# Optimization experiments

Measured on AMD Instinct MI355X. Metric: run time of the kernel, lower is better.

## Reference

```python
import jax, jax.numpy as jnp
import numpy as np

N, C_IN, C_OUT, P, W, H = 32, 32, 16, 4, 16, 16
D = P * P
EPS = 1e-6


def squash(s, axis=-1):
    # v = ||s||^2/(1+||s||^2) * s/||s||, eps-stabilized as in the repo (eps=1e-6)
    n2 = jnp.sum(s * s, axis=axis, keepdims=True)
    n = jnp.sqrt(n2)
    return (n2 / (1.0 + n2)) * s / (n + EPS)


def setup_inputs() -> dict:
    key = jax.random.key(0)
    k1, k2, k3 = jax.random.split(key, 3)
    l = jax.random.normal(k1, (N, C_IN, D, W, H), jnp.float32)
    g = jax.random.normal(k2, (N, C_OUT, D), jnp.float32)
    weight = jax.random.normal(k3, (1, C_IN, 1, C_OUT, P, P), jnp.float32)
    return {"l": l, "g": g, "weight": weight, "num_iters": 3}


def reference(l, g, weight, num_iters):
    n, c, d, w, h = l.shape
    p = weight.shape[-1]
    c_out = weight.shape[3]
    # (N, C, D, W, H) -> (N, C, W*H, P, P)
    lp = jnp.transpose(l, (0, 1, 3, 4, 2)).reshape(n, c, w * h, p, p)
    # votes: pose matmul against per-(in,out) transform matrices
    # v[n,c,s,o] = lp[n,c,s] @ weight[0,c,0,o]   -> (N, C, WH, C_out, P, P)
    v = jnp.einsum('ncsij,cojk->ncsoik', lp, weight[0, :, 0])
    M = c * w * h
    v = v.reshape(n, M, c_out, d)          # (N, M, C_out, D)
    g = g[:, None, :, :]                    # (N, 1, C_out, D)
    # dynamic routing, logits initialized from agreement with the prior global capsule g
    b = jnp.sum(v * g, axis=-1, keepdims=True)   # (N, M, C_out, 1)
    cc = None
    for _ in range(num_iters):
        cc = jax.nn.softmax(b, axis=1)           # attention over input votes M
        g = squash(jnp.sum(cc * v, axis=1, keepdims=True))  # (N, 1, C_out, D)
        b = b + jnp.sum(v * g, axis=-1, keepdims=True)
    a = jnp.squeeze(cc, -1)   # (N, M, C_out)
    g = jnp.squeeze(g, 1)     # (N, C_out, D)
    return a, g
```

## Files before the change

### kernel.cpp

```cpp
#include <hip/hip_runtime.h>
#include <math.h>

#define N_   32
#define CIN  32
#define COUT 16
#define D_   16
#define S_   256
#define M_   (CIN * S_)

#define LOG2E 1.4426950408889634f

#define PROW 20
#define PIDX(n, c, o) ((((size_t)(n) * CIN + (c)) * COUT + (o)) * PROW)

#define WS_PB0 0
#define WS_PB1 (N_ * CIN * COUT * PROW)
#define WS_G1  (2 * N_ * CIN * COUT * PROW)

#define SW(s) ((((s) & 3)) ^ (((s) >> 2) & 3))

__device__ __forceinline__ void stage_tile(const float* __restrict__ gsrc,
                                           float* ls, int tid) {
  const float4* src = (const float4*)gsrc;
#pragma unroll
  for (int j = 0; j < 4; j++) {
    int f = ((tid & 3) << 6) + (tid >> 2) + (j << 8);
    float4 val = src[f];
    int dd = f >> 6;
    int u  = f & 63;
    int chunk = dd >> 2, lo = dd & 3;
    float vv[4] = {val.x, val.y, val.z, val.w};
#pragma unroll
    for (int m = 0; m < 4; m++) {
      int s = (u << 2) + m;
      int p = chunk ^ SW(s);
      ls[(s << 4) + (p << 2) + lo] = vv[m];
    }
  }
}

__device__ __forceinline__ void read_lp(const float* ls, int s, float* lp) {
  const float4* row = (const float4*)(ls + (s << 4));
  int sw = SW(s);
#pragma unroll
  for (int c = 0; c < 4; c++) {
    float4 q = row[c ^ sw];
    lp[c * 4 + 0] = q.x; lp[c * 4 + 1] = q.y;
    lp[c * 4 + 2] = q.z; lp[c * 4 + 3] = q.w;
  }
}

__device__ __forceinline__ float dot16(const float* a, const float* b) {
  float a0 = 0.f, a1 = 0.f, a2 = 0.f, a3 = 0.f;
#pragma unroll
  for (int k = 0; k < 4; k++) {
    a0 = fmaf(a[k],      b[k],      a0);
    a1 = fmaf(a[4 + k],  b[4 + k],  a1);
    a2 = fmaf(a[8 + k],  b[8 + k],  a2);
    a3 = fmaf(a[12 + k], b[12 + k], a3);
  }
  return (a0 + a1) + (a2 + a3);
}

__global__ __launch_bounds__(256, 3) void pass_kernel(
    const float* __restrict__ l, const float* __restrict__ wgt,
    const float* __restrict__ gprev, const float* __restrict__ part_in,
    float* __restrict__ gstore, float* __restrict__ part_out,
    float* __restrict__ edump, int mode) {
  const int bid = blockIdx.x;
  const int n = bid >> 5;
  const int c = bid & 31;
  const int tid = threadIdx.x;
  const int o = tid & 15;
  const int strip = tid >> 4;

  __shared__ float ls[D_ * S_];
  __shared__ float red[4][18][16];
  __shared__ float red2[18][16];
  __shared__ float hd[16][20];

  if (mode && tid < 64) {
    const int ho = tid & 15, hs = tid >> 4;
    float H[18];
#pragma unroll
    for (int f = 0; f < 17; f++) H[f] = 0.f;
    H[17] = -INFINITY;
#pragma unroll 2
    for (int q = 0; q < 8; q++) {
      const float* r = part_in + PIDX(n, hs + 4 * q, ho);
      const float4* r4 = (const float4*)r;
#pragma unroll
      for (int i = 0; i < 4; i++) {
        float4 v = r4[i];
        H[i * 4 + 0] += v.x; H[i * 4 + 1] += v.y;
        H[i * 4 + 2] += v.z; H[i * 4 + 3] += v.w;
      }
      H[16] += r[16];
      H[17] = fmaxf(H[17], r[17]);
    }
#pragma unroll
    for (int off = 16; off <= 32; off <<= 1) {
#pragma unroll
      for (int f = 0; f < 17; f++) H[f] += __shfl_xor(H[f], off);
      H[17] = fmaxf(H[17], __shfl_xor(H[17], off));
    }
    if (tid < 16) {
      float inv = 1.0f / H[16], n2 = 0.f, Sg[16];
#pragma unroll
      for (int d = 0; d < 16; d++) { Sg[d] = H[d] * inv; n2 = fmaf(Sg[d], Sg[d], n2); }
      float coef = n2 / ((1.f + n2) * (sqrtf(n2) + 1e-6f));
      float4* hq = (float4*)hd[tid];
#pragma unroll
      for (int i = 0; i < 4; i++)
        hq[i] = make_float4(coef * Sg[i * 4 + 0], coef * Sg[i * 4 + 1],
                            coef * Sg[i * 4 + 2], coef * Sg[i * 4 + 3]);
      hd[tid][16] = H[17];
    }
  }

  stage_tile(l + ((size_t)(n * CIN + c)) * D_ * S_, ls, tid);

  float Greg[16];
  {
    const float4* gp = (const float4*)(gprev + (n * COUT + o) * 16);
#pragma unroll
    for (int i = 0; i < 4; i++) {
      float4 u = gp[i];
      Greg[i * 4 + 0] = u.x; Greg[i * 4 + 1] = u.y;
      Greg[i * 4 + 2] = u.z; Greg[i * 4 + 3] = u.w;
    }
  }

  __syncthreads();

  float shift = 0.f;
  if (mode) {
    const float4* hq = (const float4*)hd[o];
#pragma unroll
    for (int i = 0; i < 4; i++) {
      float4 v = hq[i];
      Greg[i * 4 + 0] += v.x; Greg[i * 4 + 1] += v.y;
      Greg[i * 4 + 2] += v.z; Greg[i * 4 + 3] += v.w;
    }
    shift = hd[o][16];
    if (mode == 1 && c == 0 && tid < 16) {
      float* gs = gstore + (n * COUT + tid) * 16;
      const float4* hp = (const float4*)hd[tid];
      const float4* gp = (const float4*)(gprev + (n * COUT + tid) * 16);
      float4* g4 = (float4*)gs;
#pragma unroll
      for (int i = 0; i < 4; i++) {
        float4 a = gp[i], b = hp[i];
        g4[i] = make_float4(a.x + b.x, a.y + b.y, a.z + b.z, a.w + b.w);
      }
    }
  }

  float WG[16];
  {
    float wreg[16];
    const float4* wp = (const float4*)(wgt + (c * COUT + o) * 16);
#pragma unroll
    for (int i = 0; i < 4; i++) {
      float4 t = wp[i];
      wreg[i * 4 + 0] = t.x; wreg[i * 4 + 1] = t.y;
      wreg[i * 4 + 2] = t.z; wreg[i * 4 + 3] = t.w;
    }
#pragma unroll
    for (int i = 0; i < 4; i++)
#pragma unroll
      for (int j = 0; j < 4; j++) {
        float acc = 0.f;
#pragma unroll
        for (int k = 0; k < 4; k++)
          acc = fmaf(wreg[j * 4 + k], Greg[i * 4 + k], acc);
        WG[i * 4 + j] = acc * LOG2E;
      }
  }

  float se = 0.f, bmx = -INFINITY, E[16];
#pragma unroll
  for (int d = 0; d < 16; d++) E[d] = 0.f;

#pragma unroll 4
  for (int it = 0; it < 16; it++) {
    float lp[16];
    read_lp(ls, strip + (it << 4), lp);
    float b = dot16(lp, WG) - shift;
    float e = exp2f(b);
    if (mode == 2) {
      edump[((size_t)(n * M_ + c * S_ + strip + (it << 4))) * COUT + o] = e;
    }
    bmx = fmaxf(bmx, b);
    se += e;
#pragma unroll
    for (int d = 0; d < 16; d++) E[d] = fmaf(e, lp[d], E[d]);
  }

#pragma unroll
  for (int off = 16; off <= 32; off <<= 1) {
    se += __shfl_xor(se, off);
    bmx = fmaxf(bmx, __shfl_xor(bmx, off));
#pragma unroll
    for (int d = 0; d < 16; d++) E[d] += __shfl_xor(E[d], off);
  }

  const int w = tid >> 6;
  if ((tid & 63) < 16) {
#pragma unroll
    for (int d = 0; d < 16; d++) red[w][d][o] = E[d];
    red[w][16][o] = se;
    red[w][17][o] = bmx;
  }
  __syncthreads();

  for (int p = tid; p < 288; p += 256) {
    int f = p >> 4, oo = p & 15;
    float v0 = red[0][f][oo], v1 = red[1][f][oo];
    float v2 = red[2][f][oo], v3 = red[3][f][oo];
    red2[f][oo] = (f == 17) ? fmaxf(fmaxf(v0, v1), fmaxf(v2, v3))
                            : ((v0 + v1) + (v2 + v3));
  }
  __syncthreads();

  if (tid < 16) {
    float wt[16];
    const float4* wp = (const float4*)(wgt + (c * COUT + tid) * 16);
#pragma unroll
    for (int i = 0; i < 4; i++) {
      float4 t = wp[i];
      wt[i * 4 + 0] = t.x; wt[i * 4 + 1] = t.y;
      wt[i * 4 + 2] = t.z; wt[i * 4 + 3] = t.w;
    }
    float Et[16];
#pragma unroll
    for (int d = 0; d < 16; d++) Et[d] = red2[d][tid];
    float* p0 = part_out + PIDX(n, c, tid);
    float4* p4 = (float4*)p0;
#pragma unroll
    for (int i = 0; i < 4; i++) {
      float s0 = 0.f, s1 = 0.f, s2 = 0.f, s3 = 0.f;
#pragma unroll
      for (int j = 0; j < 4; j++) {
        s0 = fmaf(Et[i * 4 + j], wt[j * 4 + 0], s0);
        s1 = fmaf(Et[i * 4 + j], wt[j * 4 + 1], s1);
        s2 = fmaf(Et[i * 4 + j], wt[j * 4 + 2], s2);
        s3 = fmaf(Et[i * 4 + j], wt[j * 4 + 3], s3);
      }
      p4[i] = make_float4(s0, s1, s2, s3);
    }
    p0[16] = red2[16][tid];
    p0[17] = red2[17][tid] + shift;
  }
}

__global__ __launch_bounds__(256, 4) void a_kernel(
    const float* __restrict__ part, float* __restrict__ a_out,
    float* __restrict__ g_out) {
  const int bid = blockIdx.x;
  const int n = bid >> 6;
  const int chunk = bid & 63;
  const int tid = threadIdx.x;

  __shared__ float sinv[16];

  if (tid < 16) {
    float se = 0.f;
    if (chunk == 0) {
      float S[16];
#pragma unroll
      for (int d = 0; d < 16; d++) S[d] = 0.f;
#pragma unroll 4
      for (int c = 0; c < CIN; c++) {
        const float* r = part + PIDX(n, c, tid);
        const float4* r4 = (const float4*)r;
#pragma unroll
        for (int i = 0; i < 4; i++) {
          float4 v = r4[i];
          S[i * 4 + 0] += v.x; S[i * 4 + 1] += v.y;
          S[i * 4 + 2] += v.z; S[i * 4 + 3] += v.w;
        }
        se += r[16];
      }
      float inv = 1.0f / se, n2 = 0.f;
#pragma unroll
      for (int d = 0; d < 16; d++) { S[d] *= inv; n2 = fmaf(S[d], S[d], n2); }
      float coef = n2 / ((1.f + n2) * (sqrtf(n2) + 1e-6f));
      float* go = g_out + (n * COUT + tid) * 16;
#pragma unroll
      for (int d = 0; d < 16; d++) go[d] = coef * S[d];
      sinv[tid] = inv;
    } else {
#pragma unroll 8
      for (int c = 0; c < CIN; c++) se += part[PIDX(n, c, tid) + 16];
      sinv[tid] = 1.0f / se;
    }
  }
  __syncthreads();

  float4* pv = (float4*)(a_out + (size_t)n * (M_ * COUT) + (size_t)chunk * 2048);
#pragma unroll
  for (int r = 0; r < 2; r++) {
    int i4 = tid + (r << 8);
    int o0 = (i4 & 3) << 2;
    float4 v = pv[i4];
    v.x *= sinv[o0 + 0];
    v.y *= sinv[o0 + 1];
    v.z *= sinv[o0 + 2];
    v.w *= sinv[o0 + 3];
    pv[i4] = v;
  }
}

extern "C" void kernel_launch(void* const* d_in, const int* in_sizes, int n_in,
                              void* d_out, int out_size, void* d_ws, size_t ws_size,
                              hipStream_t stream) {
  const float* l = (const float*)d_in[0];
  const float* g = (const float*)d_in[1];
  const float* w = (const float*)d_in[2];

  float* out = (float*)d_out;
  float* ws = (float*)d_ws;
  float* a_out = out;
  float* g_out = out + (size_t)N_ * M_ * COUT;

  float* PB0 = ws + WS_PB0;
  float* PB1 = ws + WS_PB1;
  float* G1  = ws + WS_G1;

  pass_kernel<<<N_ * CIN, 256, 0, stream>>>(l, w, g, nullptr, nullptr, PB0,
                                            nullptr, 0);
  pass_kernel<<<N_ * CIN, 256, 0, stream>>>(l, w, g, PB0, G1, PB1,
                                            nullptr, 1);
  pass_kernel<<<N_ * CIN, 256, 0, stream>>>(l, w, G1, PB1, nullptr, PB0,
                                            a_out, 2);
  a_kernel<<<N_ * 64, 256, 0, stream>>>(PB0, a_out, g_out);
}
```

Before: 119.8 us.

## Process two input channels per block with prefetch of the second tile

Each pass block now handles two input channels (c0 and c0+16), halving the grid. The second channel's tile is loaded into registers while the first is being swept, then written to shared memory after the first reduction. This hides global load latency and amortizes the per-block head reduction (mode>0) over two channels. The a_kernel likewise processes twice as many elements per block. The cost is fewer blocks (512 on a large GPU, possibly under-filling it) and higher register pressure.

```diff
diff --git a/kernel.cpp b/kernel.cpp
--- a/kernel.cpp
+++ b/kernel.cpp
@@ -19,17 +19,23 @@
 
 #define SW(s) ((((s) & 3)) ^ (((s) >> 2) & 3))
 
-__device__ __forceinline__ void stage_tile(const float* __restrict__ gsrc,
-                                           float* ls, int tid) {
+__device__ __forceinline__ void stage_load(const float* __restrict__ gsrc,
+                                           int tid, float4* vals) {
   const float4* src = (const float4*)gsrc;
+#pragma unroll
+  for (int j = 0; j < 4; j++)
+    vals[j] = src[((tid & 3) << 6) + (tid >> 2) + (j << 8)];
+}
+
+__device__ __forceinline__ void stage_store(float* ls, int tid,
+                                            const float4* vals) {
 #pragma unroll
   for (int j = 0; j < 4; j++) {
     int f = ((tid & 3) << 6) + (tid >> 2) + (j << 8);
-    float4 val = src[f];
     int dd = f >> 6;
     int u  = f & 63;
     int chunk = dd >> 2, lo = dd & 3;
-    float vv[4] = {val.x, val.y, val.z, val.w};
+    float vv[4] = {vals[j].x, vals[j].y, vals[j].z, vals[j].w};
 #pragma unroll
     for (int m = 0; m < 4; m++) {
       int s = (u << 2) + m;
@@ -61,6 +67,101 @@
   }
   return (a0 + a1) + (a2 + a3);
 }
+
+__device__ __forceinline__ void make_WG(const float* __restrict__ wgt,
+                                        int c, int o, const float* Greg,
+                                        float* WG) {
+  float wreg[16];
+  const float4* wp = (const float4*)(wgt + (c * COUT + o) * 16);
+#pragma unroll
+  for (int i = 0; i < 4; i++) {
+    float4 t = wp[i];
+    wreg[i * 4 + 0] = t.x; wreg[i * 4 + 1] = t.y;
+    wreg[i * 4 + 2] = t.z; wreg[i * 4 + 3] = t.w;
+  }
+#pragma unroll
+  for (int i = 0; i < 4; i++)
+#pragma unroll
+    for (int j = 0; j < 4; j++) {
+      float acc = 0.f;
+#pragma unroll
+      for (int k = 0; k < 4; k++)
+        acc = fmaf(wreg[j * 4 + k], Greg[i * 4 + k], acc);
+      WG[i * 4 + j] = acc * LOG2E;
+    }
+}
+
+__device__ __forceinline__ void sweep(const float* ls, const float* WG,
+                                      float shift, int strip, int doDump,
+                                      float* __restrict__ edp,
+                                      float& se, float& bmx, float* E) {
+  se = 0.f; bmx = -INFINITY;
+#pragma unroll
+  for (int d = 0; d < 16; d++) E[d] = 0.f;
+#pragma unroll 4
+  for (int it = 0; it < 16; it++) {
+    float lp[16];
+    read_lp(ls, strip + (it << 4), lp);
+    float b = dot16(lp, WG) - shift;
+    float e = exp2f(b);
+    if (doDump) edp[(size_t)(it << 4) * COUT] = e;
+    bmx = fmaxf(bmx, b);
+    se += e;
+#pragma unroll
+    for (int d = 0; d < 16; d++) E[d] = fmaf(e, lp[d], E[d]);
+  }
+#pragma unroll
+  for (int off = 16; off <= 32; off <<= 1) {
+    se += __shfl_xor(se, off);
+    bmx = fmaxf(bmx, __shfl_xor(bmx, off));
+#pragma unroll
+    for (int d = 0; d < 16; d++) E[d] += __shfl_xor(E[d], off);
+  }
+}
+
+__device__ __forceinline__ void tail_store(const float* __restrict__ wgt,
+                                           int c, int o,
+                                           float (*red2)[16],
+                                           float* __restrict__ part_out,
+                                           int n, float shift) {
+  float wt[16];
+  const float4* wp = (const float4*)(wgt + (c * COUT + o) * 16);
+#pragma unroll
+  for (int i = 0; i < 4; i++) {
+    float4 t = wp[i];
+    wt[i * 4 + 0] = t.x; wt[i * 4 + 1] = t.y;
+    wt[i * 4 + 2] = t.z; wt[i * 4 + 3] = t.w;
+  }
+  float Et[16];
+#pragma unroll
+  for (int d = 0; d < 16; d++) Et[d] = red2[d][o];
+  float* p0 = part_out + PIDX(n, c, o);
+  float4* p4 = (float4*)p0;
+#pragma unroll
+  for (int i = 0; i < 4; i++) {
+    float s0 = 0.f, s1 = 0.f, s2 = 0.f, s3 = 0.f;
+#pragma unroll
+    for (int j = 0; j < 4; j++) {
+      s0 = fmaf(Et[i * 4 + j], wt[j * 4 + 0], s0);
+      s1 = fmaf(Et[i * 4 + j], wt[j * 4 + 1], s1);
+      s2 = fmaf(Et[i * 4 + j], wt[j * 4 + 2], s2);
+      s3 = fmaf(Et[i * 4 + j], wt[j * 4 + 3], s3);
+    }
+    p4[i] = make_float4(s0, s1, s2, s3);
+  }
+  p0[16] = red2[16][o];
+  p0[17] = red2[17][o] + shift;
+}
+
+#define MERGE_STORE(w_, o_, E_, se_, bmx_)           \
+  do {                                               \
+    if ((tid & 63) < 16) {                           \
+      _Pragma("unroll")                              \
+      for (int d = 0; d < 16; d++) red[w_][d][o_] = E_[d]; \
+      red[w_][16][o_] = se_;                         \
+      red[w_][17][o_] = bmx_;                        \
+    }                                                \
+  } while (0)
 
 __global__ __launch_bounds__(256, 3) void pass_kernel(
     const float* __restrict__ l, const float* __restrict__ wgt,
@@ -68,11 +169,13 @@
     float* __restrict__ gstore, float* __restrict__ part_out,
     float* __restrict__ edump, int mode) {
   const int bid = blockIdx.x;
-  const int n = bid >> 5;
-  const int c = bid & 31;
+  const int n  = bid >> 4;
+  const int c0 = bid & 15;
+  const int c1 = c0 + 16;
   const int tid = threadIdx.x;
   const int o = tid & 15;
   const int strip = tid >> 4;
+  const int w = tid >> 6;
 
   __shared__ float ls[D_ * S_];
   __shared__ float red[4][18][16];
@@ -118,7 +221,11 @@
     }
   }
 
-  stage_tile(l + ((size_t)(n * CIN + c)) * D_ * S_, ls, tid);
+  {
+    float4 va[4];
+    stage_load(l + ((size_t)(n * CIN + c0)) * D_ * S_, tid, va);
+    stage_store(ls, tid, va);
+  }
 
   float Greg[16];
   {
@@ -143,11 +250,10 @@
       Greg[i * 4 + 2] += v.z; Greg[i * 4 + 3] += v.w;
     }
     shift = hd[o][16];
-    if (mode == 1 && c == 0 && tid < 16) {
-      float* gs = gstore + (n * COUT + tid) * 16;
+    if (mode == 1 && c0 == 0 && tid < 16) {
       const float4* hp = (const float4*)hd[tid];
       const float4* gp = (const float4*)(gprev + (n * COUT + tid) * 16);
-      float4* g4 = (float4*)gs;
+      float4* g4 = (float4*)(gstore + (n * COUT + tid) * 16);
 #pragma unroll
       for (int i = 0; i < 4; i++) {
         float4 a = gp[i], b = hp[i];
@@ -156,63 +262,22 @@
     }
   }
 
+  float4 vb[4];
+  stage_load(l + ((size_t)(n * CIN + c1)) * D_ * S_, tid, vb);
+
   float WG[16];
+  make_WG(wgt, c0, o, Greg, WG);
+  float se, bmx, E[16];
   {
-    float wreg[16];
-    const float4* wp = (const float4*)(wgt + (c * COUT + o) * 16);
-#pragma unroll
-    for (int i = 0; i < 4; i++) {
-      float4 t = wp[i];
-      wreg[i * 4 + 0] = t.x; wreg[i * 4 + 1] = t.y;
-      wreg[i * 4 + 2] = t.z; wreg[i * 4 + 3] = t.w;
-    }
-#pragma unroll
-    for (int i = 0; i < 4; i++)
-#pragma unroll
-      for (int j = 0; j < 4; j++) {
-        float acc = 0.f;
-#pragma unroll
-        for (int k = 0; k < 4; k++)
-          acc = fmaf(wreg[j * 4 + k], Greg[i * 4 + k], acc);
-        WG[i * 4 + j] = acc * LOG2E;
-      }
-  }
-
-  float se = 0.f, bmx = -INFINITY, E[16];
-#pragma unroll
-  for (int d = 0; d < 16; d++) E[d] = 0.f;
-
-#pragma unroll 4
-  for (int it = 0; it < 16; it++) {
-    float lp[16];
-    read_lp(ls, strip + (it << 4), lp);
-    float b = dot16(lp, WG) - shift;
-    float e = exp2f(b);
-    if (mode == 2) {
-      edump[((size_t)(n * M_ + c * S_ + strip + (it << 4))) * COUT + o] = e;
-    }
-    bmx = fmaxf(bmx, b);
-    se += e;
-#pragma unroll
-    for (int d = 0; d < 16; d++) E[d] = fmaf(e, lp[d], E[d]);
-  }
-
-#pragma unroll
-  for (int off = 16; off <= 32; off <<= 1) {
-    se += __shfl_xor(se, off);
-    bmx = fmaxf(bmx, __shfl_xor(bmx, off));
-#pragma unroll
-    for (int d = 0; d < 16; d++) E[d] += __shfl_xor(E[d], off);
-  }
-
-  const int w = tid >> 6;
-  if ((tid & 63) < 16) {
-#pragma unroll
-    for (int d = 0; d < 16; d++) red[w][d][o] = E[d];
-    red[w][16][o] = se;
-    red[w][17][o] = bmx;
-  }
-  __syncthreads();
+    float* edp = edump
+        ? edump + ((size_t)(n * M_ + c0 * S_ + strip)) * COUT + o : nullptr;
+    sweep(ls, WG, shift, strip, edump != nullptr, edp, se, bmx, E);
+  }
+
+  MERGE_STORE(w, o, E, se, bmx);
+  __syncthreads();
+
+  stage_store(ls, tid, vb);
 
   for (int p = tid; p < 288; p += 256) {
     int f = p >> 4, oo = p & 15;
@@ -223,43 +288,36 @@
   }
   __syncthreads();
 
-  if (tid < 16) {
-    float wt[16];
-    const float4* wp = (const float4*)(wgt + (c * COUT + tid) * 16);
-#pragma unroll
-    for (int i = 0; i < 4; i++) {
-      float4 t = wp[i];
-      wt[i * 4 + 0] = t.x; wt[i * 4 + 1] = t.y;
-      wt[i * 4 + 2] = t.z; wt[i * 4 + 3] = t.w;
-    }
-    float Et[16];
-#pragma unroll
-    for (int d = 0; d < 16; d++) Et[d] = red2[d][tid];
-    float* p0 = part_out + PIDX(n, c, tid);
-    float4* p4 = (float4*)p0;
-#pragma unroll
-    for (int i = 0; i < 4; i++) {
-      float s0 = 0.f, s1 = 0.f, s2 = 0.f, s3 = 0.f;
-#pragma unroll
-      for (int j = 0; j < 4; j++) {
-        s0 = fmaf(Et[i * 4 + j], wt[j * 4 + 0], s0);
-        s1 = fmaf(Et[i * 4 + j], wt[j * 4 + 1], s1);
-        s2 = fmaf(Et[i * 4 + j], wt[j * 4 + 2], s2);
-        s3 = fmaf(Et[i * 4 + j], wt[j * 4 + 3], s3);
-      }
-      p4[i] = make_float4(s0, s1, s2, s3);
-    }
-    p0[16] = red2[16][tid];
-    p0[17] = red2[17][tid] + shift;
-  }
+  if (tid < 16) tail_store(wgt, c0, tid, red2, part_out, n, shift);
+
+  make_WG(wgt, c1, o, Greg, WG);
+  {
+    float* edp = edump
+        ? edump + ((size_t)(n * M_ + c1 * S_ + strip)) * COUT + o : nullptr;
+    sweep(ls, WG, shift, strip, edump != nullptr, edp, se, bmx, E);
+  }
+
+  MERGE_STORE(w, o, E, se, bmx);
+  __syncthreads();
+
+  for (int p = tid; p < 288; p += 256) {
+    int f = p >> 4, oo = p & 15;
+    float v0 = red[0][f][oo], v1 = red[1][f][oo];
+    float v2 = red[2][f][oo], v3 = red[3][f][oo];
+    red2[f][oo] = (f == 17) ? fmaxf(fmaxf(v0, v1), fmaxf(v2, v3))
+                            : ((v0 + v1) + (v2 + v3));
+  }
+  __syncthreads();
+
+  if (tid < 16) tail_store(wgt, c1, tid, red2, part_out, n, shift);
 }
 
 __global__ __launch_bounds__(256, 4) void a_kernel(
     const float* __restrict__ part, float* __restrict__ a_out,
     float* __restrict__ g_out) {
   const int bid = blockIdx.x;
-  const int n = bid >> 6;
-  const int chunk = bid & 63;
+  const int n = bid >> 5;
+  const int chunk = bid & 31;
   const int tid = threadIdx.x;
 
   __shared__ float sinv[16];
@@ -298,9 +356,9 @@
   }
   __syncthreads();
 
-  float4* pv = (float4*)(a_out + (size_t)n * (M_ * COUT) + (size_t)chunk * 2048);
-#pragma unroll
-  for (int r = 0; r < 2; r++) {
+  float4* pv = (float4*)(a_out + (size_t)n * (M_ * COUT) + (size_t)chunk * 4096);
+#pragma unroll
+  for (int r = 0; r < 4; r++) {
     int i4 = tid + (r << 8);
     int o0 = (i4 & 3) << 2;
     float4 v = pv[i4];
@@ -328,11 +386,11 @@
   float* PB1 = ws + WS_PB1;
   float* G1  = ws + WS_G1;
 
-  pass_kernel<<<N_ * CIN, 256, 0, stream>>>(l, w, g, nullptr, nullptr, PB0,
-                                            nullptr, 0);
-  pass_kernel<<<N_ * CIN, 256, 0, stream>>>(l, w, g, PB0, G1, PB1,
-                                            nullptr, 1);
-  pass_kernel<<<N_ * CIN, 256, 0, stream>>>(l, w, G1, PB1, nullptr, PB0,
-                                            a_out, 2);
-  a_kernel<<<N_ * 64, 256, 0, stream>>>(PB0, a_out, g_out);
-}
+  pass_kernel<<<N_ * 16, 256, 0, stream>>>(l, w, g, nullptr, nullptr, PB0,
+                                           nullptr, 0);
+  pass_kernel<<<N_ * 16, 256, 0, stream>>>(l, w, g, PB0, G1, PB1,
+                                           nullptr, 1);
+  pass_kernel<<<N_ * 16, 256, 0, stream>>>(l, w, G1, PB1, nullptr, PB0,
+                                           a_out, 2);
+  a_kernel<<<N_ * 32, 256, 0, stream>>>(PB0, a_out, g_out);
+}
```

After: 120.8 us. About the same (+0.8%).
